# Optimization experiments

Measured on AMD Instinct MI355X. Metric: run time of the kernel, lower is better.

The kernel has to match this reference:

```python
import jax, jax.numpy as jnp
import numpy as np

DEPTH, DIM, M_DIM, K = 3, 16, 16, 8  # depth, emb_dim, EGNN m_dim default, num_nearest_neighbors
LN_EPS = 1e-5


def _gather(x, idx):
    # x: [B,L,...], idx: [B,L,K] -> [B,L,K,...] (per-batch neighbor gather)
    return jax.vmap(lambda xb, ib: xb[ib])(x, idx)


def _lin(k, fi, fo):
    k1, k2 = jax.random.split(k)
    lim = 1.0 / np.sqrt(fi)
    w = jax.random.uniform(k1, (fi, fo), minval=-lim, maxval=lim, dtype=jnp.float32)
    b = jax.random.uniform(k2, (fo,), minval=-lim, maxval=lim, dtype=jnp.float32)
    return w, b


def _stacked(k, fi, fo):
    ws, bs = zip(*[_lin(kk, fi, fo) for kk in jax.random.split(k, DEPTH)])
    return jnp.stack(ws), jnp.stack(bs)


def setup_inputs() -> dict:
    key = jax.random.key(0)
    ks = jax.random.split(key, 16)
    B, L, num_tokens = 16, 1024, 2
    edge_in = 2 * DIM + 1  # feats_i, feats_j, rel_dist
    inp = {}
    inp['coords'] = jax.random.normal(ks[0], (B, L, 3), dtype=jnp.float32) * 3.0
    inp['residues'] = jax.random.randint(ks[1], (B, L), 0, num_tokens)
    inp['lengths'] = jax.random.randint(ks[2], (B,), L // 2, L + 1)
    inp['token_emb'] = jax.random.normal(ks[3], (num_tokens, DIM), dtype=jnp.float32)
    inp['pos_emb'] = jax.random.normal(ks[4], (L, DIM), dtype=jnp.float32)
    inp['edge_w1'], inp['edge_b1'] = _stacked(ks[5], edge_in, edge_in * 2)
    inp['edge_w2'], inp['edge_b2'] = _stacked(ks[6], edge_in * 2, M_DIM)
    inp['coors_w1'], inp['coors_b1'] = _stacked(ks[7], M_DIM, M_DIM * 4)
    inp['coors_w2'], inp['coors_b2'] = _stacked(ks[8], M_DIM * 4, 1)
    inp['ln_g'] = jnp.ones((DEPTH, DIM), jnp.float32)
    inp['ln_b'] = jnp.zeros((DEPTH, DIM), jnp.float32)
    inp['node_w1'], inp['node_b1'] = _stacked(ks[9], DIM + M_DIM, DIM * 2)
    inp['node_w2'], inp['node_b2'] = _stacked(ks[10], DIM * 2, DIM)
    inp['final_w'], inp['final_b'] = _lin(ks[11], DIM, 3)
    return inp


def reference(coords, residues, lengths, token_emb, pos_emb,
              edge_w1, edge_b1, edge_w2, edge_b2,
              coors_w1, coors_b1, coors_w2, coors_b2,
              ln_g, ln_b, node_w1, node_b1, node_w2, node_b2,
              final_w, final_b):
    B, L, _ = coords.shape
    silu = jax.nn.silu
    mask = jnp.arange(L)[None, :] < lengths[:, None]                 # [B,L]
    pair_mask = mask[:, :, None] & mask[:, None, :]                  # [B,L,L]
    eye = jnp.eye(L, dtype=bool)
    # chain adjacency: i <-> i+1 where both endpoints are within length
    r = jnp.arange(L - 1)
    chain = jnp.zeros((L, L), bool).at[r, r + 1].set(True)
    chain = chain | chain.T
    adj = (chain[None] & pair_mask) & ~eye                           # [B,L,L]

    feats = token_emb[residues] + pos_emb[None, :L]                  # [B,L,D]
    coors = coords
    for d in range(DEPTH):
        # pairwise squared distances for kNN ranking (memory-bound)
        rel_dist_full = jnp.sum((coors[:, :, None] - coors[:, None, :]) ** 2, -1)  # [B,L,L]
        ranking = jnp.where(pair_mask, rel_dist_full, 1e5)
        ranking = jnp.where(eye, -1.0, ranking)   # self always selected first
        ranking = jnp.where(adj, 0.0, ranking)    # adjacency edges forced in
        _, idx = jax.lax.top_k(-ranking, K)                           # [B,L,K] smallest
        mask_j = _gather(mask, idx)
        emask = mask[:, :, None] & mask_j                             # [B,L,K] (valid_radius=inf)
        coors_j = _gather(coors, idx)                                 # [B,L,K,3]
        rel_coors = coors[:, :, None] - coors_j                       # [B,L,K,3]
        rel_dist = jnp.sum(rel_coors ** 2, -1, keepdims=True)         # [B,L,K,1]
        feats_j = _gather(feats, idx)                                 # [B,L,K,D]
        feats_i = jnp.broadcast_to(feats[:, :, None], feats_j.shape)
        edge_in = jnp.concatenate([feats_i, feats_j, rel_dist], -1)   # [B,L,K,2D+1]
        h = silu(edge_in @ edge_w1[d] + edge_b1[d])
        m_ij = silu(h @ edge_w2[d] + edge_b2[d])                      # [B,L,K,M]
        # equivariant coordinate update
        w = silu(m_ij @ coors_w1[d] + coors_b1[d]) @ coors_w2[d] + coors_b2[d]
        w = jnp.where(emask[..., None], w, 0.0)[..., 0]               # [B,L,K]
        coors = coors + jnp.einsum('blk,blkc->blc', w, rel_coors)
        # node update (norm_feats=True in EGNN_Network -> LayerNorm)
        m_i = jnp.sum(jnp.where(emask[..., None], m_ij, 0.0), 2)      # [B,L,M]
        mu = feats.mean(-1, keepdims=True)
        var = jnp.mean((feats - mu) ** 2, -1, keepdims=True)
        normed = (feats - mu) / jnp.sqrt(var + LN_EPS) * ln_g[d] + ln_b[d]
        nin = jnp.concatenate([normed, m_i], -1)                      # [B,L,D+M]
        feats = feats + (silu(nin @ node_w1[d] + node_b1[d]) @ node_w2[d] + node_b2[d])
    delta = feats @ final_w + final_b                                 # [B,L,3]
    return delta
```

## Files before the change

### kernel.cpp

```cpp
#include <hip/hip_runtime.h>
#include <math.h>

typedef unsigned long long u64;
typedef unsigned int u32;

#define NB 16
#define SL 1024
#define DIM 16
#define MDIM 16
#define KNN 8
#define CH 64
#define NHID 32
#define LN_EPS 1e-5f
#define PST 144

__device__ __forceinline__ float silu_f(float x) {
    const float e = __expf(-x);
    return x * __builtin_amdgcn_rcpf(1.0f + e);
}

__global__ __launch_bounds__(256) void init_kernel(
    const float* __restrict__ coords, const int* __restrict__ residues,
    const float* __restrict__ token_emb, const float* __restrict__ pos_emb,
    const float* __restrict__ w1tp, const float* __restrict__ g_eb1,
    float* __restrict__ coordsA, float* __restrict__ featsA,
    float* __restrict__ Pout)
{
    const int t = blockIdx.x * 256 + threadIdx.x;
    const int node = t >> 2;
    const int part = t & 3;
    const int l = node & (SL - 1);
    const int r = residues[node];
    float f[16];
    {
        const float4* te = (const float4*)(token_emb + (size_t)r * DIM);
        const float4* pe = (const float4*)(pos_emb + (size_t)l * DIM);
#pragma unroll
        for (int q = 0; q < 4; ++q) {
            float4 a = te[q], b4 = pe[q];
            f[4*q+0] = a.x + b4.x; f[4*q+1] = a.y + b4.y;
            f[4*q+2] = a.z + b4.z; f[4*q+3] = a.w + b4.w;
        }
    }
    if (part == 0) {
        float4* fo = (float4*)(featsA + (size_t)node * DIM);
#pragma unroll
        for (int q = 0; q < 4; ++q)
            fo[q] = make_float4(f[4*q], f[4*q+1], f[4*q+2], f[4*q+3]);
        coordsA[node * 3 + 0] = coords[node * 3 + 0];
        coordsA[node * 3 + 1] = coords[node * 3 + 1];
        coordsA[node * 3 + 2] = coords[node * 3 + 2];
    }
    const int ubase = (part & 1) * 33;
    const int wbase = (part < 2) ? 0 : 66;
    float res[36];
    res[33] = 0.f; res[34] = 0.f; res[35] = 0.f;
#pragma unroll
    for (int oo = 0; oo < 33; ++oo) {
        const int u = ubase + oo;
        const float* wr = w1tp + (wbase + u) * 16;
        float a0 = (part < 2) ? g_eb1[u] : 0.0f;
        float a1 = 0.f, a2 = 0.f, a3 = 0.f;
#pragma unroll
        for (int c = 0; c < 16; c += 4) {
            a0 = fmaf(f[c + 0], wr[c + 0], a0);
            a1 = fmaf(f[c + 1], wr[c + 1], a1);
            a2 = fmaf(f[c + 2], wr[c + 2], a2);
            a3 = fmaf(f[c + 3], wr[c + 3], a3);
        }
        res[oo] = (a0 + a1) + (a2 + a3);
    }
    float4* op = (float4*)(Pout + (size_t)node * PST + part * 36);
#pragma unroll
    for (int q = 0; q < 9; ++q)
        op[q] = make_float4(res[4*q], res[4*q+1], res[4*q+2], res[4*q+3]);
}

__global__ __launch_bounds__(256) void pack_kernel(
    const float* __restrict__ ew1, const float* __restrict__ ew2,
    const float* __restrict__ cw1,
    const float* __restrict__ nw1, const float* __restrict__ nw2,
    float* __restrict__ w1tp, float* __restrict__ w1rp, float* __restrict__ w2p,
    float* __restrict__ cw1t, float* __restrict__ nw1t, float* __restrict__ nw2t)
{
    const int stride = gridDim.x * 256;
    const int t0 = blockIdx.x * 256 + threadIdx.x;
    for (int idx = t0; idx < 3 * 132 * 16; idx += stride) {
        int d = idx / (132 * 16); int r = idx - d * 132 * 16; int o = r >> 4; int c = r & 15;
        int u = (o < 66) ? o : (o - 66);
        int cc = (o < 66) ? c : (16 + c);
        w1tp[idx] = ew1[(d * 33 + cc) * 66 + u];
    }
    for (int idx = t0; idx < 3 * 72; idx += stride) {
        int d = idx / 72; int o = idx - d * 72; int hh = o / 36; int uu = o - hh * 36;
        w1rp[idx] = (uu < 33) ? ew1[(d * 33 + 32) * 66 + hh * 33 + uu] : 0.0f;
    }
    for (int idx = t0; idx < 3 * 72 * 16; idx += stride) {
        int d = idx / (72 * 16); int r = idx - d * 72 * 16; int u = r >> 4; int v = r & 15;
        int hh = u / 36; int uu = u - hh * 36;
        w2p[idx] = (uu < 33) ? ew2[(d * 66 + hh * 33 + uu) * 16 + v] : 0.0f;
    }
    for (int idx = t0; idx < 3 * CH * 16; idx += stride) {
        int d = idx / (CH * 16); int r = idx - d * CH * 16; int t = r >> 4; int v = r & 15;
        cw1t[(d * CH + t) * 16 + v] = cw1[(d * 16 + v) * CH + t];
    }
    for (int idx = t0; idx < 3 * NHID * 32; idx += stride) {
        int d = idx / (NHID * 32); int r = idx - d * NHID * 32; int u = r >> 5; int c = r & 31;
        nw1t[(d * NHID + u) * 32 + c] = nw1[(d * 32 + c) * NHID + u];
    }
    for (int idx = t0; idx < 3 * 16 * 32; idx += stride) {
        int d = idx / (16 * 32); int r = idx - d * 16 * 32; int c = r >> 5; int u = r & 31;
        nw2t[(d * 16 + c) * 32 + u] = nw2[(d * 32 + u) * 16 + c];
    }
}

__device__ __forceinline__ void merge8(u32* a, const u32* bb) {
    u32 c[8];
#pragma unroll
    for (int t = 0; t < 8; ++t) c[t] = min(a[t], bb[7 - t]);
#define MCAS(x, y) { u32 mn = min(c[x], c[y]); u32 mx = max(c[x], c[y]); c[x] = mn; c[y] = mx; }
    MCAS(0, 4) MCAS(1, 5) MCAS(2, 6) MCAS(3, 7)
    MCAS(0, 2) MCAS(1, 3) MCAS(4, 6) MCAS(5, 7)
    MCAS(0, 1) MCAS(2, 3) MCAS(4, 5) MCAS(6, 7)
#undef MCAS
#pragma unroll
    for (int t = 0; t < 8; ++t) a[t] = c[t];
}

__global__ __launch_bounds__(1024) void knn_kernel(
    const float* __restrict__ coords, const int* __restrict__ lengths,
    int* __restrict__ idxbuf)
{
    __shared__ __align__(16) float4 s_cand[SL];
    __shared__ u32 lists[16][64][9];
    const int tid = threadIdx.x;
    const int b = blockIdx.x >> 4;
    const int i0 = (blockIdx.x & 15) << 6;
    const int len = lengths[b];
    const float* cb = coords + (size_t)b * SL * 3;
    for (int idx = tid; idx < SL; idx += 1024) {
        const float* cp = cb + idx * 3;
        s_cand[idx] = make_float4(cp[0], cp[1], cp[2], 0.0f);
    }
    __syncthreads();

    const int wv = tid >> 6;
    const int lane = tid & 63;
    const int i = i0 + lane;
    const bool mi = i < len;
    const float4 qi = s_cand[i];
    const float xi = qi.x, yi = qi.y, zi = qi.z;

    u32 lst[8];
#pragma unroll
    for (int t = 0; t < 8; ++t) lst[t] = 0xFFFFFFFFu;

    const int jbase = wv << 6;
#pragma unroll 4
    for (int jj = 0; jj < 64; ++jj) {
        const int j = jbase + jj;
        const float4 cj = s_cand[j];
        const float dx = xi - cj.x, dy = yi - cj.y, dz = zi - cj.z;
        const float dist = dx * dx + dy * dy + dz * dz;
        const int dij = j - i;
        const bool pm = mi && (j < len);
        const bool adjx = (dij == 1) | (dij == -1);
        float v = pm ? (adjx ? 0.0f : dist) : 1e5f;
        v = (dij == 0) ? -1.0f : v;
        u32 bits = __float_as_uint(v);
        bits ^= (u32)((int)bits >> 31) | 0x80000000u;
        const u32 key = (bits & 0xFFFFFC00u) | (u32)j;
#pragma unroll
        for (int p = 7; p >= 1; --p)
            lst[p] = min(max(key, lst[p - 1]), lst[p]);
        lst[0] = min(key, lst[0]);
    }

#pragma unroll
    for (int t = 0; t < 8; ++t) lists[wv][lane][t] = lst[t];
    __syncthreads();

    if (tid < 512) {
        const int p = tid >> 6, q = tid & 63;
        u32 a[8], bb[8];
#pragma unroll
        for (int t = 0; t < 8; ++t) { a[t] = lists[2 * p][q][t]; bb[t] = lists[2 * p + 1][q][t]; }
        merge8(a, bb);
#pragma unroll
        for (int t = 0; t < 8; ++t) lists[2 * p][q][t] = a[t];
    }
    __syncthreads();
    if (tid < 256) {
        const int p = tid >> 6, q = tid & 63;
        u32 a[8], bb[8];
#pragma unroll
        for (int t = 0; t < 8; ++t) { a[t] = lists[4 * p][q][t]; bb[t] = lists[4 * p + 2][q][t]; }
        merge8(a, bb);
#pragma unroll
        for (int t = 0; t < 8; ++t) lists[4 * p][q][t] = a[t];
    }
    __syncthreads();
    if (tid < 128) {
        const int p = tid >> 6, q = tid & 63;
        u32 a[8], bb[8];
#pragma unroll
        for (int t = 0; t < 8; ++t) { a[t] = lists[8 * p][q][t]; bb[t] = lists[8 * p + 4][q][t]; }
        merge8(a, bb);
#pragma unroll
        for (int t = 0; t < 8; ++t) lists[8 * p][q][t] = a[t];
    }
    __syncthreads();
    if (tid < 64) {
        const int q = tid;
        u32 a[8], bb[8];
#pragma unroll
        for (int t = 0; t < 8; ++t) { a[t] = lists[0][q][t]; bb[t] = lists[8][q][t]; }
        merge8(a, bb);
        const size_t node = (size_t)b * SL + i0 + q;
        int4 r0 = make_int4((int)(a[0] & 1023u), (int)(a[1] & 1023u), (int)(a[2] & 1023u), (int)(a[3] & 1023u));
        int4 r1 = make_int4((int)(a[4] & 1023u), (int)(a[5] & 1023u), (int)(a[6] & 1023u), (int)(a[7] & 1023u));
        ((int4*)idxbuf)[node * 2 + 0] = r0;
        ((int4*)idxbuf)[node * 2 + 1] = r1;
    }
}

__global__ __launch_bounds__(256, 5) void layer_kernel(
    const int d,
    const float* __restrict__ coordsIn, float* __restrict__ coordsOut,
    const float* __restrict__ featsIn, float* __restrict__ featsOut,
    const float* __restrict__ Pbuf,
    const int* __restrict__ idxbuf, const int* __restrict__ lengths,
    const float* __restrict__ w1rp, const float* __restrict__ w2p,
    const float* __restrict__ g_eb2,
    const float* __restrict__ cw1t, const float* __restrict__ g_cb1,
    const float* __restrict__ g_cw2, const float* __restrict__ g_cb2,
    const float* __restrict__ g_lng, const float* __restrict__ g_lnb,
    const float* __restrict__ nw1t, const float* __restrict__ g_nb1,
    const float* __restrict__ nw2t, const float* __restrict__ g_nb2,
    const float* __restrict__ w1tp_all, const float* __restrict__ g_eb1,
    float* __restrict__ PbufOut)
{
    __shared__ float s_w2e[72 * 16];
    __shared__ float s_w1r[72];
    __shared__ float s_cw1[CH * 16];
    __shared__ float s_cw2v[CH];
    __shared__ float s_nw1[NHID * 36];
    __shared__ float s_nw2[16 * 36];
    __shared__ float s_eb2[16], s_cb1[CH];
    __shared__ float s_lng[16], s_lnb[16], s_nb1[32], s_nb2[16];
    __shared__ float s_cb2v;
    __shared__ __align__(16) float s_ex[2 * 64 * 20];
    __shared__ __align__(16) float s_nf[16 * 20];

    const int tid = threadIdx.x;
    for (int t = tid; t < 72 * 16; t += 256) s_w2e[t] = w2p[d * 72 * 16 + t];
    for (int t = tid; t < CH * 16; t += 256) s_cw1[t] = cw1t[d * CH * 16 + t];
    for (int t = tid; t < NHID * 32; t += 256) s_nw1[(t >> 5) * 36 + (t & 31)] = nw1t[d * NHID * 32 + t];
    for (int t = tid; t < 16 * 32; t += 256) s_nw2[(t >> 5) * 36 + (t & 31)] = nw2t[d * 16 * 32 + t];
    if (tid < 72) s_w1r[tid] = w1rp[d * 72 + tid];
    if (tid < CH) { s_cw2v[tid] = g_cw2[d * CH + tid]; s_cb1[tid] = g_cb1[d * CH + tid]; }
    if (tid < 16) {
        s_eb2[tid] = g_eb2[d * 16 + tid];
        s_lng[tid] = g_lng[d * 16 + tid];
        s_lnb[tid] = g_lnb[d * 16 + tid];
        s_nb2[tid] = g_nb2[d * 16 + tid];
    }
    if (tid < 32) s_nb1[tid] = g_nb1[d * 32 + tid];
    if (tid == 0) s_cb2v = g_cb2[d];

    const int wvid = tid >> 6;
    const int h = wvid & 1;
    const int p = wvid >> 1;
    const int lane = tid & 63;
    const int e = blockIdx.x * 128 + p * 64 + lane;
    const int n = e >> 3;
    const int b = n >> 10;
    const int i = n & (SL - 1);
    const int k = lane & 7;
    const int len = lengths[b];
    const int j = idxbuf[e];
    const bool em = (i < len) && (j < len);

    float fi[16];
    {
        const float4* pp = (const float4*)(featsIn + (size_t)n * DIM);
        float4 a = pp[0], c2 = pp[1], c3 = pp[2], c4 = pp[3];
        fi[0]=a.x; fi[1]=a.y; fi[2]=a.z; fi[3]=a.w;
        fi[4]=c2.x; fi[5]=c2.y; fi[6]=c2.z; fi[7]=c2.w;
        fi[8]=c3.x; fi[9]=c3.y; fi[10]=c3.z; fi[11]=c3.w;
        fi[12]=c4.x; fi[13]=c4.y; fi[14]=c4.z; fi[15]=c4.w;
    }
    float ci[3], rel[3];
    {
        const float* cp = coordsIn + (size_t)n * 3;
        const float* cq = coordsIn + ((size_t)b * SL + j) * 3;
        ci[0] = cp[0]; ci[1] = cp[1]; ci[2] = cp[2];
        rel[0] = ci[0] - cq[0]; rel[1] = ci[1] - cq[1]; rel[2] = ci[2] - cq[2];
    }
    const float rd = fmaf(rel[0], rel[0], fmaf(rel[1], rel[1], rel[2] * rel[2]));

    const int ub = h * 36;
    const float* PiP = Pbuf + (size_t)n * PST + ub;
    const float* PjP = Pbuf + ((size_t)b * SL + j) * PST + 72 + ub;
    float4 pa = *(const float4*)PiP;
    float4 pb = *(const float4*)PjP;

    __syncthreads();

    float macc[16];
#pragma unroll
    for (int v = 0; v < 16; ++v) macc[v] = h ? 0.0f : s_eb2[v];
#pragma unroll
    for (int c4 = 0; c4 < 9; ++c4) {
        float4 na, nb;
        if (c4 < 8) {
            na = *(const float4*)(PiP + 4 * (c4 + 1));
            nb = *(const float4*)(PjP + 4 * (c4 + 1));
        }
        const int u0 = ub + c4 * 4;
        const float hu0 = silu_f(fmaf(rd, s_w1r[u0 + 0], pa.x + pb.x));
        const float hu1 = silu_f(fmaf(rd, s_w1r[u0 + 1], pa.y + pb.y));
        const float hu2 = silu_f(fmaf(rd, s_w1r[u0 + 2], pa.z + pb.z));
        const float hu3 = silu_f(fmaf(rd, s_w1r[u0 + 3], pa.w + pb.w));
        const float* w2r = &s_w2e[u0 * 16];
#pragma unroll
        for (int v = 0; v < 16; ++v) {
            float m0 = fmaf(hu0, w2r[v], macc[v]);
            float m1 = fmaf(hu1, w2r[16 + v], m0);
            float m2 = fmaf(hu2, w2r[32 + v], m1);
            macc[v] = fmaf(hu3, w2r[48 + v], m2);
        }
        if (c4 < 8) { pa = na; pb = nb; }
    }

    float4* exq = (float4*)&s_ex[((p << 6) + lane) * 20];
    if (h) {
        exq[0] = make_float4(macc[0], macc[1], macc[2], macc[3]);
        exq[1] = make_float4(macc[4], macc[5], macc[6], macc[7]);
        exq[2] = make_float4(macc[8], macc[9], macc[10], macc[11]);
        exq[3] = make_float4(macc[12], macc[13], macc[14], macc[15]);
    }
    __syncthreads();
    float mm[16];
    if (!h) {
        float4 e0 = exq[0], e1 = exq[1], e2 = exq[2], e3 = exq[3];
        macc[0]+=e0.x; macc[1]+=e0.y; macc[2]+=e0.z; macc[3]+=e0.w;
        macc[4]+=e1.x; macc[5]+=e1.y; macc[6]+=e1.z; macc[7]+=e1.w;
        macc[8]+=e2.x; macc[9]+=e2.y; macc[10]+=e2.z; macc[11]+=e2.w;
        macc[12]+=e3.x; macc[13]+=e3.y; macc[14]+=e3.z; macc[15]+=e3.w;
#pragma unroll
        for (int v = 0; v < 16; ++v) mm[v] = silu_f(macc[v]);
        exq[0] = make_float4(mm[0], mm[1], mm[2], mm[3]);
        exq[1] = make_float4(mm[4], mm[5], mm[6], mm[7]);
        exq[2] = make_float4(mm[8], mm[9], mm[10], mm[11]);
        exq[3] = make_float4(mm[12], mm[13], mm[14], mm[15]);
    }
    __syncthreads();
    if (h) {
        float4 e0 = exq[0], e1 = exq[1], e2 = exq[2], e3 = exq[3];
        mm[0]=e0.x; mm[1]=e0.y; mm[2]=e0.z; mm[3]=e0.w;
        mm[4]=e1.x; mm[5]=e1.y; mm[6]=e1.z; mm[7]=e1.w;
        mm[8]=e2.x; mm[9]=e2.y; mm[10]=e2.z; mm[11]=e2.w;
        mm[12]=e3.x; mm[13]=e3.y; mm[14]=e3.z; mm[15]=e3.w;
    }

    const int tb = h * 32;
    float wa = 0.f;
#pragma unroll 4
    for (int tt = 0; tt < 32; ++tt) {
        const float* cr = &s_cw1[(tb + tt) * 16];
        float a0 = s_cb1[tb + tt], a1 = 0.f;
#pragma unroll
        for (int v = 0; v < 16; v += 2) {
            a0 = fmaf(mm[v], cr[v], a0);
            a1 = fmaf(mm[v + 1], cr[v + 1], a1);
        }
        wa = fmaf(silu_f(a0 + a1), s_cw2v[tb + tt], wa);
    }
    s_ex[((p << 6) + lane) * 20 + 16 + h] = wa;
    __syncthreads();
    const float wao = s_ex[((p << 6) + lane) * 20 + 17 - h];
    const float we = em ? (wa + wao + s_cb2v) : 0.f;

    float wr0 = we * rel[0], wr1 = we * rel[1], wr2 = we * rel[2];
#pragma unroll
    for (int s = 1; s < 8; s <<= 1) {
        wr0 += __shfl_xor(wr0, s, 64);
        wr1 += __shfl_xor(wr1, s, 64);
        wr2 += __shfl_xor(wr2, s, 64);
    }
    if (!h && k == 0) {
        coordsOut[(size_t)n * 3 + 0] = ci[0] + wr0;
        coordsOut[(size_t)n * 3 + 1] = ci[1] + wr1;
        coordsOut[(size_t)n * 3 + 2] = ci[2] + wr2;
    }

    float mi_[16];
#pragma unroll
    for (int v = 0; v < 16; ++v) mi_[v] = em ? mm[v] : 0.f;
#pragma unroll
    for (int s = 1; s < 8; s <<= 1) {
#pragma unroll
        for (int v = 0; v < 16; ++v) mi_[v] += __shfl_xor(mi_[v], s, 64);
    }

    float mu = 0.f;
#pragma unroll
    for (int c = 0; c < 16; ++c) mu += fi[c];
    mu *= 0.0625f;
    float var = 0.f;
#pragma unroll
    for (int c = 0; c < 16; ++c) { const float dd = fi[c] - mu; var = fmaf(dd, dd, var); }
    var *= 0.0625f;
    const float rs = rsqrtf(var + LN_EPS);
    float nn[16];
#pragma unroll
    for (int c = 0; c < 16; ++c) nn[c] = fmaf((fi[c] - mu) * rs, s_lng[c], s_lnb[c]);

    float nh[4];
#pragma unroll
    for (int q = 0; q < 4; ++q) {
        const int u = k * 4 + q;
        const float* nr = &s_nw1[u * 36];
        float a0 = s_nb1[u], a1 = 0.f;
#pragma unroll
        for (int c = 0; c < 16; c += 2) {
            a0 = fmaf(nn[c], nr[c], a0);
            a1 = fmaf(nn[c + 1], nr[c + 1], a1);
        }
#pragma unroll
        for (int v = 0; v < 16; v += 2) {
            a0 = fmaf(mi_[v], nr[16 + v], a0);
            a1 = fmaf(mi_[v + 1], nr[16 + v + 1], a1);
        }
        nh[q] = silu_f(a0 + a1);
    }

    const int c0 = 2 * k, c1 = 2 * k + 1;
    const float* w2a = &s_nw2[c0 * 36];
    const float* w2b = &s_nw2[c1 * 36];
    float o0 = s_nb2[c0], o1 = s_nb2[c1];
    const int lbase = lane & ~7;
#pragma unroll
    for (int u = 0; u < 32; ++u) {
        const float v = __shfl(nh[u & 3], lbase + (u >> 2), 64);
        o0 = fmaf(v, w2a[u], o0);
        o1 = fmaf(v, w2b[u], o1);
    }
    if (!h) {
        const float fo0 = fi[c0] + o0;
        const float fo1 = fi[c1] + o1;
        ((float2*)featsOut)[(size_t)n * 8 + k] = make_float2(fo0, fo1);
        const int nl = (p << 3) + (lane >> 3);
        s_nf[nl * 20 + c0] = fo0;
        s_nf[nl * 20 + c1] = fo1;
    }

    if (d < 2) {
        __syncthreads();
        const int nl2 = tid >> 4;
        const int sub = tid & 15;
        const int gnode = blockIdx.x * 16 + nl2;
        float fr[16];
        {
            const float4* fp = (const float4*)&s_nf[nl2 * 20];
            float4 q0 = fp[0], q1 = fp[1], q2 = fp[2], q3 = fp[3];
            fr[0]=q0.x; fr[1]=q0.y; fr[2]=q0.z; fr[3]=q0.w;
            fr[4]=q1.x; fr[5]=q1.y; fr[6]=q1.z; fr[7]=q1.w;
            fr[8]=q2.x; fr[9]=q2.y; fr[10]=q2.z; fr[11]=q2.w;
            fr[12]=q3.x; fr[13]=q3.y; fr[14]=q3.z; fr[15]=q3.w;
        }
        const float* wbase = w1tp_all + (d + 1) * 132 * 16;
        const float* bbase = g_eb1 + (d + 1) * 66;
        float* Pout = PbufOut + (size_t)gnode * PST;
#pragma unroll
        for (int q = 0; q < 9; ++q) {
            const int col = sub + (q << 4);
            const int ch = (col >= 108) ? 3 : (col >= 72) ? 2 : (col >= 36) ? 1 : 0;
            const int uu = col - ch * 36;
            const bool valid = uu < 33;
            const int u = ((ch & 1) ? 33 : 0) + uu;
            const int uc = valid ? u : 0;
            const int widx = valid ? ((ch < 2) ? u : 66 + u) : 0;
            float a0 = (valid && ch < 2) ? bbase[uc] : 0.0f;
            float a1 = 0.f, a2 = 0.f, a3 = 0.f;
            const float* wr = wbase + widx * 16;
#pragma unroll
            for (int cc = 0; cc < 16; cc += 4) {
                a0 = fmaf(fr[cc + 0], wr[cc + 0], a0);
                a1 = fmaf(fr[cc + 1], wr[cc + 1], a1);
                a2 = fmaf(fr[cc + 2], wr[cc + 2], a2);
                a3 = fmaf(fr[cc + 3], wr[cc + 3], a3);
            }
            Pout[col] = valid ? ((a0 + a1) + (a2 + a3)) : 0.0f;
        }
    }
}

__global__ __launch_bounds__(256) void final_kernel(
    const float* __restrict__ feats, const float* __restrict__ fw,
    const float* __restrict__ fb, float* __restrict__ out)
{
    const int nid = blockIdx.x * 256 + threadIdx.x;
    if (nid >= NB * SL) return;
    float f[DIM];
#pragma unroll
    for (int c = 0; c < DIM; ++c) f[c] = feats[nid * DIM + c];
#pragma unroll
    for (int o = 0; o < 3; ++o) {
        float acc = fb[o];
#pragma unroll
        for (int c = 0; c < DIM; ++c) acc = fmaf(f[c], fw[c * 3 + o], acc);
        out[nid * 3 + o] = acc;
    }
}

extern "C" void kernel_launch(void* const* d_in, const int* in_sizes, int n_in,
                              void* d_out, int out_size, void* d_ws, size_t ws_size,
                              hipStream_t stream) {
    const float* coords    = (const float*)d_in[0];
    const int*   residues  = (const int*)d_in[1];
    const int*   lengths   = (const int*)d_in[2];
    const float* token_emb = (const float*)d_in[3];
    const float* pos_emb   = (const float*)d_in[4];
    const float* ew1 = (const float*)d_in[5];
    const float* eb1 = (const float*)d_in[6];
    const float* ew2 = (const float*)d_in[7];
    const float* eb2 = (const float*)d_in[8];
    const float* cw1 = (const float*)d_in[9];
    const float* cb1 = (const float*)d_in[10];
    const float* cw2 = (const float*)d_in[11];
    const float* cb2 = (const float*)d_in[12];
    const float* lng = (const float*)d_in[13];
    const float* lnb = (const float*)d_in[14];
    const float* nw1 = (const float*)d_in[15];
    const float* nb1 = (const float*)d_in[16];
    const float* nw2 = (const float*)d_in[17];
    const float* nb2 = (const float*)d_in[18];
    const float* fw  = (const float*)d_in[19];
    const float* fb  = (const float*)d_in[20];

    float* ws = (float*)d_ws;
    float* coordsA = ws;
    float* coordsB = coordsA + NB * SL * 3;
    float* featsA  = coordsB + NB * SL * 3;
    float* featsB  = featsA + NB * SL * DIM;
    int*   idxbuf  = (int*)(featsB + NB * SL * DIM);
    float* w1tp = (float*)(idxbuf + NB * SL * KNN);
    float* w1rp = w1tp + 3 * 132 * 16;
    float* w2p  = w1rp + 3 * 72;
    float* cw1t = w2p + 3 * 72 * 16;
    float* nw1t = cw1t + 3 * CH * 16;
    float* nw2t = nw1t + 3 * NHID * 32;
    float* PbufA = nw2t + 3 * 16 * 32;
    float* PbufB = PbufA + (size_t)NB * SL * PST;

    pack_kernel<<<32, 256, 0, stream>>>(ew1, ew2, cw1, nw1, nw2, w1tp, w1rp, w2p, cw1t, nw1t, nw2t);
    init_kernel<<<NB * SL * 4 / 256, 256, 0, stream>>>(coords, residues, token_emb, pos_emb,
                                                        w1tp, eb1, coordsA, featsA, PbufA);

    float* cIn = coordsA; float* cOut = coordsB;
    float* fIn = featsA;  float* fOut = featsB;
    float* pIn = PbufA;   float* pOut = PbufB;
    for (int d = 0; d < 3; ++d) {
        knn_kernel<<<NB * SL / 64, 1024, 0, stream>>>(cIn, lengths, idxbuf);
        layer_kernel<<<NB * SL * KNN / 128, 256, 0, stream>>>(d, cIn, cOut, fIn, fOut, pIn, idxbuf, lengths,
            w1rp, w2p, eb2, cw1t, cb1, cw2, cb2, lng, lnb, nw1t, nb1, nw2t, nb2,
            w1tp, eb1, pOut);
        float* t;
        t = cIn; cIn = cOut; cOut = t;
        t = fIn; fIn = fOut; fOut = t;
        t = pIn; pIn = pOut; pOut = t;
    }

    final_kernel<<<NB * SL / 256, 256, 0, stream>>>(fIn, fw, fb, (float*)d_out);
}
```

Baseline: 280.3 us.

## Remap edge halves into same wavefront and replace LDS exchanges with shuffles

Thread mapping changes so the two hidden-unit halves of each edge sit in lanes 8 apart within one wavefront, and each node occupies 16 consecutive lanes. The shared-memory exchanges and the barriers between halves become __shfl_xor, the node MLP is split across 16 lanes, and the next-layer feature broadcast uses shuffles instead of LDS. This removes several __syncthreads and about 12KB of LDS, and launch bounds are raised to 8 waves/SIMD, which may constrain registers and cause spills.

```diff
diff --git a/kernel.cpp b/kernel.cpp
--- a/kernel.cpp
+++ b/kernel.cpp
@@ -224,7 +224,7 @@
     }
 }
 
-__global__ __launch_bounds__(256, 5) void layer_kernel(
+__global__ __launch_bounds__(256, 8) void layer_kernel(
     const int d,
     const float* __restrict__ coordsIn, float* __restrict__ coordsOut,
     const float* __restrict__ featsIn, float* __restrict__ featsOut,
@@ -249,8 +249,6 @@
     __shared__ float s_eb2[16], s_cb1[CH];
     __shared__ float s_lng[16], s_lnb[16], s_nb1[32], s_nb2[16];
     __shared__ float s_cb2v;
-    __shared__ __align__(16) float s_ex[2 * 64 * 20];
-    __shared__ __align__(16) float s_nf[16 * 20];
 
     const int tid = threadIdx.x;
     for (int t = tid; t < 72 * 16; t += 256) s_w2e[t] = w2p[d * 72 * 16 + t];
@@ -268,17 +266,14 @@
     if (tid < 32) s_nb1[tid] = g_nb1[d * 32 + tid];
     if (tid == 0) s_cb2v = g_cb2[d];
 
-    const int wvid = tid >> 6;
-    const int h = wvid & 1;
-    const int p = wvid >> 1;
     const int lane = tid & 63;
-    const int e = blockIdx.x * 128 + p * 64 + lane;
-    const int n = e >> 3;
+    const int h = (lane >> 3) & 1;
+    const int k = lane & 7;
+    const int n = blockIdx.x * 16 + (tid >> 4);
     const int b = n >> 10;
     const int i = n & (SL - 1);
-    const int k = lane & 7;
     const int len = lengths[b];
-    const int j = idxbuf[e];
+    const int j = idxbuf[n * 8 + k];
     const bool em = (i < len) && (j < len);
 
     float fi[16];
@@ -333,36 +328,10 @@
         if (c4 < 8) { pa = na; pb = nb; }
     }
 
-    float4* exq = (float4*)&s_ex[((p << 6) + lane) * 20];
-    if (h) {
-        exq[0] = make_float4(macc[0], macc[1], macc[2], macc[3]);
-        exq[1] = make_float4(macc[4], macc[5], macc[6], macc[7]);
-        exq[2] = make_float4(macc[8], macc[9], macc[10], macc[11]);
-        exq[3] = make_float4(macc[12], macc[13], macc[14], macc[15]);
-    }
-    __syncthreads();
     float mm[16];
-    if (!h) {
-        float4 e0 = exq[0], e1 = exq[1], e2 = exq[2], e3 = exq[3];
-        macc[0]+=e0.x; macc[1]+=e0.y; macc[2]+=e0.z; macc[3]+=e0.w;
-        macc[4]+=e1.x; macc[5]+=e1.y; macc[6]+=e1.z; macc[7]+=e1.w;
-        macc[8]+=e2.x; macc[9]+=e2.y; macc[10]+=e2.z; macc[11]+=e2.w;
-        macc[12]+=e3.x; macc[13]+=e3.y; macc[14]+=e3.z; macc[15]+=e3.w;
-#pragma unroll
-        for (int v = 0; v < 16; ++v) mm[v] = silu_f(macc[v]);
-        exq[0] = make_float4(mm[0], mm[1], mm[2], mm[3]);
-        exq[1] = make_float4(mm[4], mm[5], mm[6], mm[7]);
-        exq[2] = make_float4(mm[8], mm[9], mm[10], mm[11]);
-        exq[3] = make_float4(mm[12], mm[13], mm[14], mm[15]);
-    }
-    __syncthreads();
-    if (h) {
-        float4 e0 = exq[0], e1 = exq[1], e2 = exq[2], e3 = exq[3];
-        mm[0]=e0.x; mm[1]=e0.y; mm[2]=e0.z; mm[3]=e0.w;
-        mm[4]=e1.x; mm[5]=e1.y; mm[6]=e1.z; mm[7]=e1.w;
-        mm[8]=e2.x; mm[9]=e2.y; mm[10]=e2.z; mm[11]=e2.w;
-        mm[12]=e3.x; mm[13]=e3.y; mm[14]=e3.z; mm[15]=e3.w;
-    }
+#pragma unroll
+    for (int v = 0; v < 16; ++v)
+        mm[v] = silu_f(macc[v] + __shfl_xor(macc[v], 8, 64));
 
     const int tb = h * 32;
     float wa = 0.f;
@@ -377,9 +346,7 @@
         }
         wa = fmaf(silu_f(a0 + a1), s_cw2v[tb + tt], wa);
     }
-    s_ex[((p << 6) + lane) * 20 + 16 + h] = wa;
-    __syncthreads();
-    const float wao = s_ex[((p << 6) + lane) * 20 + 17 - h];
+    const float wao = __shfl_xor(wa, 8, 64);
     const float we = em ? (wa + wao + s_cb2v) : 0.f;
 
     float wr0 = we * rel[0], wr1 = we * rel[1], wr2 = we * rel[2];
@@ -389,7 +356,7 @@
         wr1 += __shfl_xor(wr1, s, 64);
         wr2 += __shfl_xor(wr2, s, 64);
     }
-    if (!h && k == 0) {
+    if ((lane & 15) == 0) {
         coordsOut[(size_t)n * 3 + 0] = ci[0] + wr0;
         coordsOut[(size_t)n * 3 + 1] = ci[1] + wr1;
         coordsOut[(size_t)n * 3 + 2] = ci[2] + wr2;
@@ -417,10 +384,11 @@
 #pragma unroll
     for (int c = 0; c < 16; ++c) nn[c] = fmaf((fi[c] - mu) * rs, s_lng[c], s_lnb[c]);
 
-    float nh[4];
-#pragma unroll
-    for (int q = 0; q < 4; ++q) {
-        const int u = k * 4 + q;
+    const int sub = lane & 15;
+    float nh[2];
+#pragma unroll
+    for (int q = 0; q < 2; ++q) {
+        const int u = sub * 2 + q;
         const float* nr = &s_nw1[u * 36];
         float a0 = s_nb1[u], a1 = 0.f;
 #pragma unroll
@@ -436,43 +404,24 @@
         nh[q] = silu_f(a0 + a1);
     }
 
-    const int c0 = 2 * k, c1 = 2 * k + 1;
-    const float* w2a = &s_nw2[c0 * 36];
-    const float* w2b = &s_nw2[c1 * 36];
-    float o0 = s_nb2[c0], o1 = s_nb2[c1];
-    const int lbase = lane & ~7;
+    const int nbase = lane & ~15;
+    const float* w2c = &s_nw2[sub * 36];
+    float o0 = s_nb2[sub];
 #pragma unroll
     for (int u = 0; u < 32; ++u) {
-        const float v = __shfl(nh[u & 3], lbase + (u >> 2), 64);
-        o0 = fmaf(v, w2a[u], o0);
-        o1 = fmaf(v, w2b[u], o1);
-    }
-    if (!h) {
-        const float fo0 = fi[c0] + o0;
-        const float fo1 = fi[c1] + o1;
-        ((float2*)featsOut)[(size_t)n * 8 + k] = make_float2(fo0, fo1);
-        const int nl = (p << 3) + (lane >> 3);
-        s_nf[nl * 20 + c0] = fo0;
-        s_nf[nl * 20 + c1] = fo1;
-    }
+        const float v = __shfl(nh[u & 1], nbase + (u >> 1), 64);
+        o0 = fmaf(v, w2c[u], o0);
+    }
+    const float fo = fi[sub] + o0;
+    featsOut[(size_t)n * DIM + sub] = fo;
 
     if (d < 2) {
-        __syncthreads();
-        const int nl2 = tid >> 4;
-        const int sub = tid & 15;
-        const int gnode = blockIdx.x * 16 + nl2;
         float fr[16];
-        {
-            const float4* fp = (const float4*)&s_nf[nl2 * 20];
-            float4 q0 = fp[0], q1 = fp[1], q2 = fp[2], q3 = fp[3];
-            fr[0]=q0.x; fr[1]=q0.y; fr[2]=q0.z; fr[3]=q0.w;
-            fr[4]=q1.x; fr[5]=q1.y; fr[6]=q1.z; fr[7]=q1.w;
-            fr[8]=q2.x; fr[9]=q2.y; fr[10]=q2.z; fr[11]=q2.w;
-            fr[12]=q3.x; fr[13]=q3.y; fr[14]=q3.z; fr[15]=q3.w;
-        }
+#pragma unroll
+        for (int c = 0; c < 16; ++c) fr[c] = __shfl(fo, nbase + c, 64);
         const float* wbase = w1tp_all + (d + 1) * 132 * 16;
         const float* bbase = g_eb1 + (d + 1) * 66;
-        float* Pout = PbufOut + (size_t)gnode * PST;
+        float* Pout = PbufOut + (size_t)n * PST;
 #pragma unroll
         for (int q = 0; q < 9; ++q) {
             const int col = sub + (q << 4);
```

Measured after the change: 310.3 us. 1.11x slower.
